# Performance work log

Measured on AMD Instinct MI355X. Metric: run time of the kernel, lower is better.

The kernel has to match this reference:

```python
import jax, jax.numpy as jnp
import numpy as np

N_PROTS = 20000
N_GRAPHS = 16
N = N_PROTS * N_GRAPHS        # 320_000 nodes
F = 128                       # input features
L = 10                        # lat_size (hard-coded in module)
E = 10_240_000                # edges, avg degree 32


def setup_inputs() -> dict:
    key = jax.random.key(0)
    ks = jax.random.split(key, 8)
    x = jax.random.normal(ks[0], (N, F), dtype=jnp.float32)
    edge_index = jax.random.randint(ks[1], (2, E), 0, N, dtype=jnp.int32)
    def lin(k, fan_in, shape):
        return jax.random.uniform(k, shape, jnp.float32, -1.0, 1.0) / np.sqrt(fan_in)
    return {
        "x": x,
        "edge_index": edge_index,
        "W_in": lin(ks[2], F, (F, L)),
        "b_in": jnp.zeros((L,), jnp.float32),
        "W1": lin(ks[3], L, (L, L)),
        "b1": jnp.zeros((L,), jnp.float32),
        "W2": lin(ks[4], L, (L, L)),
        "b2": jnp.zeros((L,), jnp.float32),
        "W_out": lin(ks[5], L, (L, 1)),
        "b_out": jnp.zeros((1,), jnp.float32),
    }


def _gcn_improved(h, row, col, deg_inv_sqrt, W, b):
    # GCNConv(improved=True): A_hat = A + 2I, out = D^-1/2 A_hat D^-1/2 (h W) + b
    hw = h @ W                                   # [N, L]
    norm = deg_inv_sqrt[row] * deg_inv_sqrt[col]  # [E]
    agg = jax.ops.segment_sum(norm[:, None] * hw[row], col, num_segments=N)
    # self-loop with weight 2: contributes 2/deg * hw per node
    agg = agg + (2.0 * deg_inv_sqrt * deg_inv_sqrt)[:, None] * hw
    return agg + b


def reference(x, edge_index, W_in, b_in, W1, b1, W2, b2, W_out, b_out):
    row, col = edge_index[0], edge_index[1]
    # degree incl. self-loop fill value 2.0 (improved)
    deg = jax.ops.segment_sum(jnp.ones((E,), jnp.float32), col, num_segments=N) + 2.0
    deg_inv_sqrt = jax.lax.rsqrt(deg)

    h = jax.nn.relu(x @ W_in + b_in)                         # input_linear + relu
    h = jax.nn.relu(_gcn_improved(h, row, col, deg_inv_sqrt, W1, b1))
    h = jax.nn.relu(_gcn_improved(h, row, col, deg_inv_sqrt, W2, b2))
    out = h @ W_out + b_out                                  # output_linear
    return out.reshape(-1, N_PROTS, 1)
```

## Files before the change

kernel.cpp:

```cpp
#include <hip/hip_runtime.h>

#define NN 320000
#define FF 128
#define EE 10240000
#define NBUK 625
#define CSH 9
#define CLOC 512
#define BCAP2 17280
#define SLABDIV 20000u
#define KEYS 8192
#define EPB 40000

__global__ __launch_bounds__(1024) void k_bucket(const int* __restrict__ row,
                                                 const int* __restrict__ col,
                                                 int* __restrict__ gcur,
                                                 int* __restrict__ buf) {
  __shared__ int hist[NBUK];
  __shared__ int cur[NBUK];
  int t = threadIdx.x;
  long long e0 = (long long)blockIdx.x * EPB;

  for (int b = t; b < NBUK; b += 1024) hist[b] = 0;
  __syncthreads();

  for (int i = t; i < EPB; i += 1024) {
    atomicAdd(&hist[col[e0 + i] >> CSH], 1);
  }
  __syncthreads();

  for (int b = t; b < NBUK; b += 1024) {
    cur[b] = atomicAdd(&gcur[b], hist[b]);
  }
  __syncthreads();

  for (int i = t; i < EPB; i += 1024) {
    int c = col[e0 + i];
    int r = row[e0 + i];
    int b = c >> CSH;
    int slot = atomicAdd(&cur[b], 1);
    if (slot < BCAP2) buf[(long long)b * BCAP2 + slot] = (r << CSH) | (c & (CLOC - 1));
  }
}

__global__ __launch_bounds__(512) void k_sortdeg(const int* __restrict__ gcur,
                                                 int* __restrict__ buf,
                                                 int* __restrict__ off,
                                                 float* __restrict__ dis) {
  __shared__ int stage[BCAP2];
  __shared__ int hist[KEYS];
  __shared__ int tsum[512];
  int t = threadIdx.x;
  int b = blockIdx.x;
  long long base = (long long)b * BCAP2;
  int cnt = gcur[b]; if (cnt > BCAP2) cnt = BCAP2;

#pragma unroll
  for (int k = 0; k < 16; k++) hist[t * 16 + k] = 0;
  __syncthreads();

  for (int i = t; i < cnt; i += 512) {
    int e = buf[base + i];
    stage[i] = e;
    int key = ((e & (CLOC - 1)) << 4) | (int)((unsigned)(e >> CSH) / SLABDIV);
    atomicAdd(&hist[key], 1);
  }
  __syncthreads();

  int mysum = 0;
#pragma unroll
  for (int k = 0; k < 16; k++) mysum += hist[t * 16 + k];
  tsum[t] = mysum;
  __syncthreads();
  for (int o = 1; o < 512; o <<= 1) {
    int v = (t >= o) ? tsum[t - o] : 0;
    __syncthreads();
    tsum[t] += v;
    __syncthreads();
  }
  int runbase = tsum[t] - mysum;
  int running = runbase;
#pragma unroll
  for (int k = 0; k < 16; k++) {
    int old = hist[t * 16 + k];
    hist[t * 16 + k] = running;
    running += old;
  }
  off[b * 513 + t] = runbase;
  if (t == 0) off[b * 513 + 512] = cnt;
  dis[b * CLOC + t] = rsqrtf((float)mysum + 2.0f);
  __syncthreads();

  for (int i = t; i < cnt; i += 512) {
    int e = stage[i];
    int key = ((e & (CLOC - 1)) << 4) | (int)((unsigned)(e >> CSH) / SLABDIV);
    int slot = atomicAdd(&hist[key], 1);
    buf[base + slot] = e >> CSH;
  }
}

__global__ __launch_bounds__(256) void k_h0(const float* __restrict__ x,
                                            const float* __restrict__ Win,
                                            const float* __restrict__ bin,
                                            const float* __restrict__ W1,
                                            const float* __restrict__ dis,
                                            float* __restrict__ g1) {
  int n = blockIdx.x * 256 + threadIdx.x;
  float acc[10];
#pragma unroll
  for (int l = 0; l < 10; l++) acc[l] = bin[l];

  const float4* xr = (const float4*)(x + (long long)n * FF);
#pragma unroll
  for (int j = 0; j < FF / 4; j++) {
    float4 v = xr[j];
    const float* w = Win + (j * 4) * 10;
#pragma unroll
    for (int l = 0; l < 10; l++) acc[l] = fmaf(v.x, w[l], acc[l]);
#pragma unroll
    for (int l = 0; l < 10; l++) acc[l] = fmaf(v.y, w[10 + l], acc[l]);
#pragma unroll
    for (int l = 0; l < 10; l++) acc[l] = fmaf(v.z, w[20 + l], acc[l]);
#pragma unroll
    for (int l = 0; l < 10; l++) acc[l] = fmaf(v.w, w[30 + l], acc[l]);
  }
  float h[10];
#pragma unroll
  for (int l = 0; l < 10; l++) h[l] = fmaxf(acc[l], 0.f);

  float hw[10];
#pragma unroll
  for (int l = 0; l < 10; l++) hw[l] = 0.f;
#pragma unroll
  for (int k = 0; k < 10; k++) {
    const float* wr = W1 + k * 10;
#pragma unroll
    for (int l = 0; l < 10; l++) hw[l] = fmaf(h[k], wr[l], hw[l]);
  }

  float di = dis[n];
  float4* gp = (float4*)(g1 + (long long)n * 12);
  gp[0] = make_float4(di * hw[0], di * hw[1], di * hw[2], di * hw[3]);
  gp[1] = make_float4(di * hw[4], di * hw[5], di * hw[6], di * hw[7]);
  gp[2] = make_float4(di * hw[8], di * hw[9], 0.f, 0.f);
}

#define GATHER_RUN(GSRC)                                             \
  for (int i = s; i < e; i++) {                                      \
    int r = __builtin_nontemporal_load(bb + i);                      \
    const float4* q = (const float4*)(GSRC + (long long)r * 12);     \
    float4 A = q[0], B = q[1];                                       \
    float2 C = *(const float2*)(q + 2);                              \
    acc[0] += A.x; acc[1] += A.y; acc[2] += A.z; acc[3] += A.w;      \
    acc[4] += B.x; acc[5] += B.y; acc[6] += B.z; acc[7] += B.w;      \
    acc[8] += C.x; acc[9] += C.y;                                    \
  }

__global__ __launch_bounds__(256) void k_scatter_mid(const int* __restrict__ buf,
                                                     const int* __restrict__ off,
                                                     const float* __restrict__ g1,
                                                     const float* __restrict__ dis,
                                                     const float* __restrict__ b1,
                                                     const float* __restrict__ W2,
                                                     float* __restrict__ g2) {
  int n = blockIdx.x * 256 + threadIdx.x;
  int b = n >> CSH;
  int c = n & (CLOC - 1);
  const int* bb = buf + (long long)b * BCAP2;
  int s = off[b * 513 + c];
  int e = off[b * 513 + c + 1];

  float acc[10];
#pragma unroll
  for (int l = 0; l < 10; l++) acc[l] = 0.f;
  GATHER_RUN(g1);

  float di = dis[n];
  float tw = 2.0f * di;
  const float4* g1p = (const float4*)(g1 + (long long)n * 12);
  float4 ga = g1p[0], gb = g1p[1];
  float2 gc = *(const float2*)(g1p + 2);

  float h[10];
  h[0] = fmaxf(fmaf(di, acc[0], fmaf(tw, ga.x, b1[0])), 0.f);
  h[1] = fmaxf(fmaf(di, acc[1], fmaf(tw, ga.y, b1[1])), 0.f);
  h[2] = fmaxf(fmaf(di, acc[2], fmaf(tw, ga.z, b1[2])), 0.f);
  h[3] = fmaxf(fmaf(di, acc[3], fmaf(tw, ga.w, b1[3])), 0.f);
  h[4] = fmaxf(fmaf(di, acc[4], fmaf(tw, gb.x, b1[4])), 0.f);
  h[5] = fmaxf(fmaf(di, acc[5], fmaf(tw, gb.y, b1[5])), 0.f);
  h[6] = fmaxf(fmaf(di, acc[6], fmaf(tw, gb.z, b1[6])), 0.f);
  h[7] = fmaxf(fmaf(di, acc[7], fmaf(tw, gb.w, b1[7])), 0.f);
  h[8] = fmaxf(fmaf(di, acc[8], fmaf(tw, gc.x, b1[8])), 0.f);
  h[9] = fmaxf(fmaf(di, acc[9], fmaf(tw, gc.y, b1[9])), 0.f);

  float hw[10];
#pragma unroll
  for (int l = 0; l < 10; l++) hw[l] = 0.f;
#pragma unroll
  for (int k = 0; k < 10; k++) {
    const float* wr = W2 + k * 10;
#pragma unroll
    for (int l = 0; l < 10; l++) hw[l] = fmaf(h[k], wr[l], hw[l]);
  }

  float4* gp = (float4*)(g2 + (long long)n * 12);
  gp[0] = make_float4(di * hw[0], di * hw[1], di * hw[2], di * hw[3]);
  gp[1] = make_float4(di * hw[4], di * hw[5], di * hw[6], di * hw[7]);
  gp[2] = make_float4(di * hw[8], di * hw[9], 0.f, 0.f);
}

__global__ __launch_bounds__(256) void k_scatter_out(const int* __restrict__ buf,
                                                     const int* __restrict__ off,
                                                     const float* __restrict__ g2,
                                                     const float* __restrict__ dis,
                                                     const float* __restrict__ b2,
                                                     const float* __restrict__ Wout,
                                                     const float* __restrict__ bout,
                                                     float* __restrict__ out) {
  int n = blockIdx.x * 256 + threadIdx.x;
  int b = n >> CSH;
  int c = n & (CLOC - 1);
  const int* bb = buf + (long long)b * BCAP2;
  int s = off[b * 513 + c];
  int e = off[b * 513 + c + 1];

  float acc[10];
#pragma unroll
  for (int l = 0; l < 10; l++) acc[l] = 0.f;
  GATHER_RUN(g2);

  float di = dis[n];
  float tw = 2.0f * di;
  const float4* g2p = (const float4*)(g2 + (long long)n * 12);
  float4 ga = g2p[0], gb = g2p[1];
  float2 gc = *(const float2*)(g2p + 2);

  float h[10];
  h[0] = fmaxf(fmaf(di, acc[0], fmaf(tw, ga.x, b2[0])), 0.f);
  h[1] = fmaxf(fmaf(di, acc[1], fmaf(tw, ga.y, b2[1])), 0.f);
  h[2] = fmaxf(fmaf(di, acc[2], fmaf(tw, ga.z, b2[2])), 0.f);
  h[3] = fmaxf(fmaf(di, acc[3], fmaf(tw, ga.w, b2[3])), 0.f);
  h[4] = fmaxf(fmaf(di, acc[4], fmaf(tw, gb.x, b2[4])), 0.f);
  h[5] = fmaxf(fmaf(di, acc[5], fmaf(tw, gb.y, b2[5])), 0.f);
  h[6] = fmaxf(fmaf(di, acc[6], fmaf(tw, gb.z, b2[6])), 0.f);
  h[7] = fmaxf(fmaf(di, acc[7], fmaf(tw, gb.w, b2[7])), 0.f);
  h[8] = fmaxf(fmaf(di, acc[8], fmaf(tw, gc.x, b2[8])), 0.f);
  h[9] = fmaxf(fmaf(di, acc[9], fmaf(tw, gc.y, b2[9])), 0.f);

  float o = bout[0];
#pragma unroll
  for (int l = 0; l < 10; l++) o = fmaf(h[l], Wout[l], o);
  out[n] = o;
}

extern "C" void kernel_launch(void* const* d_in, const int* in_sizes, int n_in,
                              void* d_out, int out_size, void* d_ws, size_t ws_size,
                              hipStream_t stream) {
  const float* x    = (const float*)d_in[0];
  const int*   ei   = (const int*)d_in[1];
  const float* Win  = (const float*)d_in[2];
  const float* bin  = (const float*)d_in[3];
  const float* W1   = (const float*)d_in[4];
  const float* b1   = (const float*)d_in[5];
  const float* W2   = (const float*)d_in[6];
  const float* b2   = (const float*)d_in[7];
  const float* Wout = (const float*)d_in[8];
  const float* bout = (const float*)d_in[9];
  float* out = (float*)d_out;

  int*   buf  = (int*)d_ws;
  int*   gcur = buf + (long long)NBUK * BCAP2;
  int*   off  = gcur + 1024;
  float* dis  = (float*)(off + NBUK * 513);
  float* g1   = dis + NN;
  float* g2   = g1 + 12 * NN;

  const int* row = ei;
  const int* col = ei + EE;

  hipMemsetAsync(gcur, 0, NBUK * sizeof(int), stream);
  k_bucket<<<256, 1024, 0, stream>>>(row, col, gcur, buf);
  k_sortdeg<<<NBUK, 512, 0, stream>>>(gcur, buf, off, dis);
  k_h0<<<NN / 256, 256, 0, stream>>>(x, Win, bin, W1, dis, g1);
  k_scatter_mid<<<NN / 256, 256, 0, stream>>>(buf, off, g1, dis, b1, W2, g2);
  k_scatter_out<<<NN / 256, 256, 0, stream>>>(buf, off, g2, dis, b2, Wout, bout, out);
}
```

Measured before the change: 1.126 ms.

## Gather in block-synchronized source slabs with 64-byte padded feature rows

Cuts the source-slab sort key from 16 slabs to 8 and pads the per-node g1/g2 feature rows from 12 to 16 floats, so each row sits in one 64-byte aligned segment. The gather loop now walks the sorted neighbor list slab by slab and calls __syncthreads after each slab. This keeps the threads of a block reading from the same source range at roughly the same time, which should improve L2 locality. The cost is eight barriers per thread, larger g buffers, and an extra index load at each slab boundary. The dis offset also changes to a fixed constant.

```diff
diff --git a/kernel.cpp b/kernel.cpp
--- a/kernel.cpp
+++ b/kernel.cpp
@@ -7,9 +7,11 @@
 #define CSH 9
 #define CLOC 512
 #define BCAP2 17280
-#define SLABDIV 20000u
-#define KEYS 8192
+#define NSLAB 8
+#define SLABDIV 40000u
+#define KEYS 4096
 #define EPB 40000
+#define GSTRIDE 16
 
 __global__ __launch_bounds__(1024) void k_bucket(const int* __restrict__ row,
                                                  const int* __restrict__ col,
@@ -55,20 +57,20 @@
   int cnt = gcur[b]; if (cnt > BCAP2) cnt = BCAP2;
 
 #pragma unroll
-  for (int k = 0; k < 16; k++) hist[t * 16 + k] = 0;
+  for (int k = 0; k < NSLAB; k++) hist[t * NSLAB + k] = 0;
   __syncthreads();
 
   for (int i = t; i < cnt; i += 512) {
     int e = buf[base + i];
     stage[i] = e;
-    int key = ((e & (CLOC - 1)) << 4) | (int)((unsigned)(e >> CSH) / SLABDIV);
+    int key = ((e & (CLOC - 1)) << 3) | (int)((unsigned)(e >> CSH) / SLABDIV);
     atomicAdd(&hist[key], 1);
   }
   __syncthreads();
 
   int mysum = 0;
 #pragma unroll
-  for (int k = 0; k < 16; k++) mysum += hist[t * 16 + k];
+  for (int k = 0; k < NSLAB; k++) mysum += hist[t * NSLAB + k];
   tsum[t] = mysum;
   __syncthreads();
   for (int o = 1; o < 512; o <<= 1) {
@@ -80,9 +82,9 @@
   int runbase = tsum[t] - mysum;
   int running = runbase;
 #pragma unroll
-  for (int k = 0; k < 16; k++) {
-    int old = hist[t * 16 + k];
-    hist[t * 16 + k] = running;
+  for (int k = 0; k < NSLAB; k++) {
+    int old = hist[t * NSLAB + k];
+    hist[t * NSLAB + k] = running;
     running += old;
   }
   off[b * 513 + t] = runbase;
@@ -92,7 +94,7 @@
 
   for (int i = t; i < cnt; i += 512) {
     int e = stage[i];
-    int key = ((e & (CLOC - 1)) << 4) | (int)((unsigned)(e >> CSH) / SLABDIV);
+    int key = ((e & (CLOC - 1)) << 3) | (int)((unsigned)(e >> CSH) / SLABDIV);
     int slot = atomicAdd(&hist[key], 1);
     buf[base + slot] = e >> CSH;
   }
@@ -138,21 +140,30 @@
   }
 
   float di = dis[n];
-  float4* gp = (float4*)(g1 + (long long)n * 12);
+  float4* gp = (float4*)(g1 + (long long)n * GSTRIDE);
   gp[0] = make_float4(di * hw[0], di * hw[1], di * hw[2], di * hw[3]);
   gp[1] = make_float4(di * hw[4], di * hw[5], di * hw[6], di * hw[7]);
   gp[2] = make_float4(di * hw[8], di * hw[9], 0.f, 0.f);
 }
 
 #define GATHER_RUN(GSRC)                                             \
-  for (int i = s; i < e; i++) {                                      \
-    int r = __builtin_nontemporal_load(bb + i);                      \
-    const float4* q = (const float4*)(GSRC + (long long)r * 12);     \
-    float4 A = q[0], B = q[1];                                       \
-    float2 C = *(const float2*)(q + 2);                              \
-    acc[0] += A.x; acc[1] += A.y; acc[2] += A.z; acc[3] += A.w;      \
-    acc[4] += B.x; acc[5] += B.y; acc[6] += B.z; acc[7] += B.w;      \
-    acc[8] += C.x; acc[9] += C.y;                                    \
+  {                                                                  \
+    int i = s;                                                       \
+    for (int k = 0; k < NSLAB; k++) {                                \
+      int bound = (k + 1) * (int)SLABDIV;                            \
+      while (i < e) {                                                \
+        int r = __builtin_nontemporal_load(bb + i);                  \
+        if (r >= bound) break;                                       \
+        const float4* q = (const float4*)(GSRC + (long long)r * GSTRIDE); \
+        float4 A = q[0], B = q[1];                                   \
+        float2 C = *(const float2*)(q + 2);                          \
+        acc[0] += A.x; acc[1] += A.y; acc[2] += A.z; acc[3] += A.w;  \
+        acc[4] += B.x; acc[5] += B.y; acc[6] += B.z; acc[7] += B.w;  \
+        acc[8] += C.x; acc[9] += C.y;                                \
+        i++;                                                         \
+      }                                                              \
+      __syncthreads();                                               \
+    }                                                                \
   }
 
 __global__ __launch_bounds__(256) void k_scatter_mid(const int* __restrict__ buf,
@@ -176,7 +187,7 @@
 
   float di = dis[n];
   float tw = 2.0f * di;
-  const float4* g1p = (const float4*)(g1 + (long long)n * 12);
+  const float4* g1p = (const float4*)(g1 + (long long)n * GSTRIDE);
   float4 ga = g1p[0], gb = g1p[1];
   float2 gc = *(const float2*)(g1p + 2);
 
@@ -202,7 +213,7 @@
     for (int l = 0; l < 10; l++) hw[l] = fmaf(h[k], wr[l], hw[l]);
   }
 
-  float4* gp = (float4*)(g2 + (long long)n * 12);
+  float4* gp = (float4*)(g2 + (long long)n * GSTRIDE);
   gp[0] = make_float4(di * hw[0], di * hw[1], di * hw[2], di * hw[3]);
   gp[1] = make_float4(di * hw[4], di * hw[5], di * hw[6], di * hw[7]);
   gp[2] = make_float4(di * hw[8], di * hw[9], 0.f, 0.f);
@@ -230,7 +241,7 @@
 
   float di = dis[n];
   float tw = 2.0f * di;
-  const float4* g2p = (const float4*)(g2 + (long long)n * 12);
+  const float4* g2p = (const float4*)(g2 + (long long)n * GSTRIDE);
   float4 ga = g2p[0], gb = g2p[1];
   float2 gc = *(const float2*)(g2p + 2);
 
@@ -270,9 +281,9 @@
   int*   buf  = (int*)d_ws;
   int*   gcur = buf + (long long)NBUK * BCAP2;
   int*   off  = gcur + 1024;
-  float* dis  = (float*)(off + NBUK * 513);
+  float* dis  = (float*)(off + 321024);
   float* g1   = dis + NN;
-  float* g2   = g1 + 12 * NN;
+  float* g2   = g1 + GSTRIDE * NN;
 
   const int* row = ei;
   const int* col = ei + EE;
```

New measurement: 1.074 ms. -4.6%, faster.
